# Performance work log

Hardware: AMD Instinct MI355X
Metric: run time of the kernel (lower is better)

The kernel has to match this reference:

```python
import jax, jax.numpy as jnp
import numpy as np

N_EMBD = 768
N_HEAD = 8
B, T = 4, 2048

def setup_inputs() -> dict:
    key = jax.random.key(0)
    k1, k2, k3, k4, k5 = jax.random.split(key, 5)
    C = N_EMBD
    s = 1.0 / np.sqrt(C)
    return {
        "x": jax.random.normal(k1, (B, T, C), dtype=jnp.float32),
        "W_attn": jax.random.normal(k2, (C, 3 * C), dtype=jnp.float32) * s,
        "b_attn": jnp.zeros((3 * C,), dtype=jnp.float32),
        "W_proj": jax.random.normal(k3, (C, C), dtype=jnp.float32) * s,
        "b_proj": jnp.zeros((C,), dtype=jnp.float32),
    }

def reference(x, W_attn, b_attn, W_proj, b_proj):
    Bs, Ts, C = x.shape
    H = N_HEAD
    hs = C // H
    qkv = x @ W_attn + b_attn                      # [B,T,3C]
    q, k, v = jnp.split(qkv, 3, axis=-1)
    # reshape to [B,H,T,hs]
    q = q.reshape(Bs, Ts, H, hs).transpose(0, 2, 1, 3)
    k = k.reshape(Bs, Ts, H, hs).transpose(0, 2, 1, 3)
    v = v.reshape(Bs, Ts, H, hs).transpose(0, 2, 1, 3)
    scale = 1.0 / jnp.sqrt(jnp.float32(hs))
    att = jnp.einsum('bhid,bhjd->bhij', q, k) * scale   # [B,H,T,T]
    mask = jnp.tril(jnp.ones((Ts, Ts), dtype=bool))
    att = jnp.where(mask, att, -jnp.inf)
    m = jnp.max(att, axis=-1, keepdims=True)
    e = jnp.where(mask, jnp.exp(att - m), 0.0)
    # original kernel divides by (sum + 1e-9)
    att = e / (jnp.sum(e, axis=-1, keepdims=True) + 1e-9)
    y = jnp.einsum('bhij,bhjd->bhid', att, v)           # [B,H,T,hs]
    y = y.transpose(0, 2, 1, 3).reshape(Bs, Ts, C)
    return y @ W_proj + b_proj
```

## Files before the change

kernel.cpp:

```cpp
#include <hip/hip_runtime.h>

typedef __bf16 bf16;
typedef __attribute__((ext_vector_type(4))) __bf16 bf16x4;
typedef __attribute__((ext_vector_type(8))) __bf16 bf16x8;
typedef __attribute__((ext_vector_type(4))) float f32x4;

#define B_   4
#define T_   2048
#define C_   768
#define H_   8
#define HS_  96
#define M_   (B_ * T_)
#define QKN_ (3 * C_)

#define NEG_BIG (-1e30f)

#define KSTR 104
#define VSTR 72

__device__ __forceinline__ void gload_lds16(const bf16* g, bf16* l) {
    __builtin_amdgcn_global_load_lds(
        (const __attribute__((address_space(1))) uint32_t*)g,
        (__attribute__((address_space(3))) uint32_t*)l,
        16, 0, 0);
}

__device__ __forceinline__ bf16x8 cvt8(f32x4 v0, f32x4 v1) {
    bf16x8 o;
#pragma unroll
    for (int i = 0; i < 4; ++i) { o[i] = (bf16)v0[i]; o[4 + i] = (bf16)v1[i]; }
    return o;
}

__global__ void transpose_kernel(const float* __restrict__ W, bf16* __restrict__ Wt,
                                 int R, int Cn) {
    __shared__ bf16 tile[32][33];
    int tx = threadIdx.x, ty = threadIdx.y;
    int x  = blockIdx.x * 32 + tx;
    int y0 = blockIdx.y * 32;
#pragma unroll
    for (int j = 0; j < 32; j += 8)
        tile[ty + j][tx] = (bf16)W[(size_t)(y0 + ty + j) * Cn + x];
    __syncthreads();
    int y2 = blockIdx.x * 32;
    int x2 = y0 + tx;
#pragma unroll
    for (int j = 0; j < 32; j += 8)
        Wt[(size_t)(y2 + ty + j) * R + x2] = tile[tx][ty + j];
}

__global__ void sentinel_kernel(float* __restrict__ out, int n) {
    int i = blockIdx.x * 256 + threadIdx.x;
    if (i < n) out[i] = 12345.0f;
}

__global__ __launch_bounds__(256) void convert_bf16_kernel(const float* __restrict__ in,
                                                           bf16* __restrict__ out,
                                                           int n8) {
    int i = blockIdx.x * 256 + threadIdx.x;
    if (i >= n8) return;
    const float* p = in + (size_t)i * 8;
    f32x4 a = *(const f32x4*)p;
    f32x4 b = *(const f32x4*)(p + 4);
    *(bf16x8*)&out[(size_t)i * 8] = cvt8(a, b);
}

#define CONV_BLKS (M_ * C_ / 8 / 256)
#define TA_BX (QKN_ / 32)
#define TA_BLKS (TA_BX * (C_ / 32))
#define TP_BX (C_ / 32)
#define TP_BLKS (TP_BX * (C_ / 32))

__device__ __forceinline__ void transpose_body(bf16 (*tile)[33],
                                               const float* __restrict__ W,
                                               bf16* __restrict__ Wt,
                                               int R, int Cn, int bx, int by, int tid) {
    int tx = tid & 31, ty = tid >> 5;
    int x  = bx * 32 + tx;
    int y0 = by * 32;
#pragma unroll
    for (int j = 0; j < 32; j += 8)
        tile[ty + j][tx] = (bf16)W[(size_t)(y0 + ty + j) * Cn + x];
    __syncthreads();
    int y2 = bx * 32;
    int x2 = y0 + tx;
#pragma unroll
    for (int j = 0; j < 32; j += 8)
        Wt[(size_t)(y2 + ty + j) * R + x2] = tile[tx][ty + j];
}

__global__ __launch_bounds__(256) void prep_kernel(const float* __restrict__ x,
                                                   bf16* __restrict__ xb,
                                                   const float* __restrict__ Wa,
                                                   bf16* __restrict__ Wta,
                                                   const float* __restrict__ Wp,
                                                   bf16* __restrict__ Wtp) {
    __shared__ bf16 tile[32][33];
    int bid = blockIdx.x;
    int tid = threadIdx.x;
    if (bid < CONV_BLKS) {
        int i = bid * 256 + tid;
        const float* p = x + (size_t)i * 8;
        f32x4 a = *(const f32x4*)p;
        f32x4 b = *(const f32x4*)(p + 4);
        *(bf16x8*)&xb[(size_t)i * 8] = cvt8(a, b);
    } else if (bid < CONV_BLKS + TA_BLKS) {
        int t = bid - CONV_BLKS;
        transpose_body(tile, Wa, Wta, C_, QKN_, t % TA_BX, t / TA_BX, tid);
    } else {
        int t = bid - CONV_BLKS - TA_BLKS;
        transpose_body(tile, Wp, Wtp, C_, C_, t % TP_BX, t / TP_BX, tid);
    }
}

#define TILE_ELEMS (128 * 64)

__global__ __launch_bounds__(256) void gemm_qkv(const bf16* __restrict__ A,
                                                const bf16* __restrict__ Bt,
                                                const float* __restrict__ bias,
                                                bf16* __restrict__ Cmat,
                                                bf16* __restrict__ Vt,
                                                int M, int N, int K) {
    __shared__ bf16 lda[2 * TILE_ELEMS];
    __shared__ bf16 ldb[2 * TILE_ELEMS];
    int tid  = threadIdx.x;
    int w    = tid >> 6;
    int lane = tid & 63;
    int col  = lane & 15, quad = lane >> 4;
    int wr   = w >> 1, wc = w & 1;
    int m0   = blockIdx.y * 128, n0 = blockIdx.x * 128;

    int srow = lane >> 3;
    int scol = (lane & 7) * 8;
    const bf16* gA[4]; const bf16* gB[4]; bf16* lA[4]; bf16* lB[4];
#pragma unroll
    for (int i = 0; i < 4; ++i) {
        int seg = w * 4 + i;
        int row = seg * 8 + srow;
        gA[i] = &A[(size_t)(m0 + row) * K + scol];
        gB[i] = &Bt[(size_t)(n0 + row) * K + scol];
        lA[i] = &lda[seg * 512];
        lB[i] = &ldb[seg * 512];
    }

    const f32x4 zero = {0.f, 0.f, 0.f, 0.f};
    f32x4 acc[4][4];
#pragma unroll
    for (int mr = 0; mr < 4; ++mr)
#pragma unroll
        for (int nc = 0; nc < 4; ++nc) acc[mr][nc] = zero;

#pragma unroll
    for (int i = 0; i < 4; ++i) {
        gload_lds16(gA[i], lA[i]);
        gload_lds16(gB[i], lB[i]);
    }
    __syncthreads();

    int cur = 0;
    for (int k0 = 0; k0 < K; k0 += 64) {
        int nxt = cur ^ 1;
        if (k0 + 64 < K) {
#pragma unroll
            for (int i = 0; i < 4; ++i) {
                gload_lds16(gA[i] + k0 + 64, lA[i] + nxt * TILE_ELEMS);
                gload_lds16(gB[i] + k0 + 64, lB[i] + nxt * TILE_ELEMS);
            }
        }
        const bf16* la = &lda[cur * TILE_ELEMS];
        const bf16* lb = &ldb[cur * TILE_ELEMS];
#pragma unroll
        for (int ks = 0; ks < 2; ++ks) {
            bf16x8 af[4], bfr[4];
#pragma unroll
            for (int t = 0; t < 4; ++t) {
                af[t]  = *(const bf16x8*)&la[(wr * 64 + t * 16 + col) * 64 + ks * 32 + quad * 8];
                bfr[t] = *(const bf16x8*)&lb[(wc * 64 + t * 16 + col) * 64 + ks * 32 + quad * 8];
            }
#pragma unroll
            for (int mr = 0; mr < 4; ++mr)
#pragma unroll
                for (int nc = 0; nc < 4; ++nc)
                    acc[mr][nc] = __builtin_amdgcn_mfma_f32_16x16x32_bf16(
                        af[mr], bfr[nc], acc[mr][nc], 0, 0, 0);
        }
        __syncthreads();
        cur = nxt;
    }

#pragma unroll
    for (int nc = 0; nc < 4; ++nc) {
        int n = n0 + wc * 64 + nc * 16 + col;
        float bv = bias[n];
#pragma unroll
        for (int mr = 0; mr < 4; ++mr) {
#pragma unroll
            for (int r = 0; r < 4; ++r) {
                int row = m0 + wr * 64 + mr * 16 + quad * 4 + r;
                Cmat[(size_t)row * N + n] = (bf16)(acc[mr][nc][r] + bv);
            }
        }
    }
    if (n0 >= 2 * C_) {
        int batch = m0 >> 11;
        bf16* Vtb = Vt + (size_t)batch * C_ * T_;
        int t0 = (m0 & 2047) + wr * 64;
#pragma unroll
        for (int nc = 0; nc < 4; ++nc) {
            int n  = n0 + wc * 64 + nc * 16 + col;
            int vc = n - 2 * C_;
            float bv = bias[n];
#pragma unroll
            for (int mr = 0; mr < 4; ++mr) {
                int t  = t0 + mr * 16 + quad * 4;
                int tb = t & ~63;
                int a  = (t >> 2) & 15;
                int ts = tb + ((a & 7) << 3) + ((a >> 3) << 2);
                bf16x4 pk = {(bf16)(acc[mr][nc][0] + bv), (bf16)(acc[mr][nc][1] + bv),
                             (bf16)(acc[mr][nc][2] + bv), (bf16)(acc[mr][nc][3] + bv)};
                *(bf16x4*)&Vtb[(size_t)vc * T_ + ts] = pk;
            }
        }
    }
}

__global__ __launch_bounds__(256) void gemm_proj(const bf16* __restrict__ A,
                                                 const bf16* __restrict__ Bt,
                                                 const float* __restrict__ bias,
                                                 float* __restrict__ Cmat,
                                                 int M, int N, int K) {
    __shared__ bf16 lda[2 * TILE_ELEMS];
    __shared__ bf16 ldb[2 * TILE_ELEMS];
    int tid  = threadIdx.x;
    int w    = tid >> 6;
    int lane = tid & 63;
    int col  = lane & 15, quad = lane >> 4;
    int wr   = w >> 1, wc = w & 1;
    int m0   = blockIdx.y * 128, n0 = blockIdx.x * 128;

    int srow = lane >> 3;
    int scol = (lane & 7) * 8;
    const bf16* gA[4]; const bf16* gB[4]; bf16* lA[4]; bf16* lB[4];
#pragma unroll
    for (int i = 0; i < 4; ++i) {
        int seg = w * 4 + i;
        int row = seg * 8 + srow;
        gA[i] = &A[(size_t)(m0 + row) * K + scol];
        gB[i] = &Bt[(size_t)(n0 + row) * K + scol];
        lA[i] = &lda[seg * 512];
        lB[i] = &ldb[seg * 512];
    }

    const f32x4 zero = {0.f, 0.f, 0.f, 0.f};
    f32x4 acc[4][4];
#pragma unroll
    for (int mr = 0; mr < 4; ++mr)
#pragma unroll
        for (int nc = 0; nc < 4; ++nc) acc[mr][nc] = zero;

#pragma unroll
    for (int i = 0; i < 4; ++i) {
        gload_lds16(gA[i], lA[i]);
        gload_lds16(gB[i], lB[i]);
    }
    __syncthreads();

    int cur = 0;
    for (int k0 = 0; k0 < K; k0 += 64) {
        int nxt = cur ^ 1;
        if (k0 + 64 < K) {
#pragma unroll
            for (int i = 0; i < 4; ++i) {
                gload_lds16(gA[i] + k0 + 64, lA[i] + nxt * TILE_ELEMS);
                gload_lds16(gB[i] + k0 + 64, lB[i] + nxt * TILE_ELEMS);
            }
        }
        const bf16* la = &lda[cur * TILE_ELEMS];
        const bf16* lb = &ldb[cur * TILE_ELEMS];
#pragma unroll
        for (int ks = 0; ks < 2; ++ks) {
            bf16x8 af[4], bfr[4];
#pragma unroll
            for (int t = 0; t < 4; ++t) {
                af[t]  = *(const bf16x8*)&la[(wr * 64 + t * 16 + col) * 64 + ks * 32 + quad * 8];
                bfr[t] = *(const bf16x8*)&lb[(wc * 64 + t * 16 + col) * 64 + ks * 32 + quad * 8];
            }
#pragma unroll
            for (int mr = 0; mr < 4; ++mr)
#pragma unroll
                for (int nc = 0; nc < 4; ++nc)
                    acc[mr][nc] = __builtin_amdgcn_mfma_f32_16x16x32_bf16(
                        af[mr], bfr[nc], acc[mr][nc], 0, 0, 0);
        }
        __syncthreads();
        cur = nxt;
    }

#pragma unroll
    for (int nc = 0; nc < 4; ++nc) {
        int n = n0 + wc * 64 + nc * 16 + col;
        float bv = bias[n];
#pragma unroll
        for (int mr = 0; mr < 4; ++mr) {
#pragma unroll
            for (int r = 0; r < 4; ++r) {
                int row = m0 + wr * 64 + mr * 16 + quad * 4 + r;
                Cmat[(size_t)row * N + n] = acc[mr][nc][r] + bv;
            }
        }
    }
}

__global__ __launch_bounds__(256) void attn_kernel(const bf16* __restrict__ qkv,
                                                   const bf16* __restrict__ Vt,
                                                   bf16* __restrict__ y,
                                                   int nGroups) {
    __shared__ bf16 ldsK[64 * KSTR];
    __shared__ bf16 ldsV[96 * VSTR];
    const int bid  = blockIdx.x;
    const int qt   = 31 - bid / nGroups;
    const int g    = bid % nGroups;
    const int h    = g & 7, b = g >> 3;
    const int tid  = threadIdx.x;
    const int w    = tid >> 6, lane = tid & 63;
    const int col  = lane & 15, quad = lane >> 4;
    const float SCALE2 = 0.10206207261596577f * 1.4426950408889634f;
    const float M0 = 24.0f;
    const f32x4 zero = {0.f, 0.f, 0.f, 0.f};

    const bf16* qkvb = qkv + (size_t)b * T_ * QKN_;
    const bf16* Vtbh = Vt + (size_t)(b * H_ + h) * HS_ * T_;
    bf16* yb  = y + (size_t)b * T_ * C_;

    const int rbase = qt * 64 + w * 16;

    bf16x8 qf[3];
#pragma unroll
    for (int c = 0; c < 3; ++c)
        qf[c] = *(const bf16x8*)&qkvb[(size_t)(rbase + col) * QKN_ + h * HS_ + c * 32 + quad * 8];

    const bf16* pK[3]; const bf16* pV[3];
    bf16 *dK[3], *dV[3];
#pragma unroll
    for (int i = 0; i < 3; ++i) {
        int chunk = i * 256 + tid;
        int rK = chunk / 12, cK = chunk - rK * 12;
        pK[i] = qkvb + (size_t)rK * QKN_ + C_ + h * HS_ + cK * 8;
        dK[i] = &ldsK[rK * KSTR + cK * 8];
        int rV = chunk >> 3, cV = chunk & 7;
        pV[i] = Vtbh + (size_t)rV * T_ + cV * 8;
        dV[i] = &ldsV[rV * VSTR + cV * 8];
    }

    f32x4 o[6];
#pragma unroll
    for (int n2 = 0; n2 < 6; ++n2) o[n2] = zero;
    f32x4 lsum4 = zero;

    bf16x8 kreg[3], vreg[3];
#pragma unroll
    for (int i = 0; i < 3; ++i) {
        kreg[i] = *(const bf16x8*)pK[i];
        vreg[i] = *(const bf16x8*)pV[i];
        pK[i] += (size_t)64 * QKN_;
        pV[i] += 64;
    }

    const int njt = qt + 1;
    for (int jt = 0; jt < njt; ++jt) {
        int jb = jt * 64;
        __syncthreads();
#pragma unroll
        for (int i = 0; i < 3; ++i) {
            *(bf16x8*)dK[i] = kreg[i];
            *(bf16x8*)dV[i] = vreg[i];
        }
        __syncthreads();
        if (jt + 1 < njt) {
#pragma unroll
            for (int i = 0; i < 3; ++i) {
                kreg[i] = *(const bf16x8*)pK[i];
                vreg[i] = *(const bf16x8*)pV[i];
                pK[i] += (size_t)64 * QKN_;
                pV[i] += 64;
            }
        }

        f32x4 st[4];
#pragma unroll
        for (int nb = 0; nb < 4; ++nb) {
            st[nb] = zero;
#pragma unroll
            for (int c = 0; c < 3; ++c) {
                bf16x8 kf = *(const bf16x8*)&ldsK[(nb * 16 + col) * KSTR + c * 32 + quad * 8];
                st[nb] = __builtin_amdgcn_mfma_f32_16x16x32_bf16(
                    kf, qf[c], st[nb], 0, 0, 0);
            }
        }

        if (jt == njt - 1) {
#pragma unroll
            for (int nb = 0; nb < 4; ++nb)
#pragma unroll
                for (int r = 0; r < 4; ++r) {
                    int jg = jb + nb * 16 + quad * 4 + r;
                    st[nb][r] = (jg <= rbase + col) ? fmaf(st[nb][r], SCALE2, -M0)
                                                    : NEG_BIG;
                }
        } else {
#pragma unroll
            for (int nb = 0; nb < 4; ++nb)
#pragma unroll
                for (int r = 0; r < 4; ++r)
                    st[nb][r] = fmaf(st[nb][r], SCALE2, -M0);
        }

#pragma unroll
        for (int nb = 0; nb < 4; ++nb) {
#pragma unroll
            for (int r = 0; r < 4; ++r)
                st[nb][r] = exp2f(st[nb][r]);
            lsum4 += st[nb];
        }

        bf16x8 palo, pahi;
#pragma unroll
        for (int r = 0; r < 4; ++r) {
            palo[r]     = (bf16)st[0][r];
            palo[4 + r] = (bf16)st[2][r];
            pahi[r]     = (bf16)st[1][r];
            pahi[4 + r] = (bf16)st[3][r];
        }

#pragma unroll
        for (int n2 = 0; n2 < 6; ++n2) {
            const bf16* vrow = &ldsV[(n2 * 16 + col) * VSTR];
            bf16x8 vlo = *(const bf16x8*)&vrow[quad * 8];
            bf16x8 vhi = *(const bf16x8*)&vrow[32 + quad * 8];
            o[n2] = __builtin_amdgcn_mfma_f32_16x16x32_bf16(vlo, palo, o[n2], 0, 0, 0);
            o[n2] = __builtin_amdgcn_mfma_f32_16x16x32_bf16(vhi, pahi, o[n2], 0, 0, 0);
        }
    }

    float lsum = (lsum4[0] + lsum4[1]) + (lsum4[2] + lsum4[3]);
    lsum += __shfl_xor(lsum, 16, 64);
    lsum += __shfl_xor(lsum, 32, 64);
    float linv = 1.0f / lsum;
#pragma unroll
    for (int n2 = 0; n2 < 6; ++n2) {
        bf16x4 pk = {(bf16)(o[n2][0] * linv), (bf16)(o[n2][1] * linv),
                     (bf16)(o[n2][2] * linv), (bf16)(o[n2][3] * linv)};
        *(bf16x4*)&yb[(size_t)(rbase + col) * C_ + h * HS_ + n2 * 16 + quad * 4] = pk;
    }
}

extern "C" void kernel_launch(void* const* d_in, const int* in_sizes, int n_in,
                              void* d_out, int out_size, void* d_ws, size_t ws_size,
                              hipStream_t stream) {
    (void)in_sizes; (void)n_in;
    const float* x      = (const float*)d_in[0];
    const float* W_attn = (const float*)d_in[1];
    const float* b_attn = (const float*)d_in[2];
    const float* W_proj = (const float*)d_in[3];
    const float* b_proj = (const float*)d_in[4];
    float* out = (float*)d_out;

    size_t e_wta = (size_t)QKN_ * C_;
    size_t e_wtp = (size_t)C_ * C_;
    size_t a_qkv = e_wta + e_wtp;
    size_t a_vt  = a_qkv + (size_t)M_ * QKN_;
    size_t a_yb  = a_vt + (size_t)M_ * C_;
    size_t needA = (a_yb + (size_t)M_ * C_) * sizeof(bf16);
    size_t b_qkv = e_wta + e_wtp;
    size_t b_vt  = b_qkv + (size_t)T_ * QKN_;
    size_t b_yb  = b_vt + (size_t)T_ * C_;
    size_t needB = (b_yb + (size_t)T_ * C_) * sizeof(bf16);

    if (ws_size >= needA) {
        bf16* Wt_attn = (bf16*)d_ws;
        bf16* Wt_proj = (bf16*)d_ws + e_wta;
        bf16* qkv     = (bf16*)d_ws + a_qkv;
        bf16* Vt      = (bf16*)d_ws + a_vt;
        bf16* yb      = (bf16*)d_ws + a_yb;
        bf16* xb      = yb;
        prep_kernel<<<dim3(CONV_BLKS + TA_BLKS + TP_BLKS), 256, 0, stream>>>(
            x, xb, W_attn, Wt_attn, W_proj, Wt_proj);
        gemm_qkv<<<dim3(QKN_ / 128, M_ / 128), 256, 0, stream>>>(
            xb, Wt_attn, b_attn, qkv, Vt, M_, QKN_, C_);
        attn_kernel<<<dim3(32 * H_ * B_), 256, 0, stream>>>(qkv, Vt, yb, H_ * B_);
        gemm_proj<<<dim3(C_ / 128, M_ / 128), 256, 0, stream>>>(
            yb, Wt_proj, b_proj, out, M_, C_, C_);
    } else if (ws_size >= needB) {
        bf16* Wt_attn = (bf16*)d_ws;
        bf16* Wt_proj = (bf16*)d_ws + e_wta;
        bf16* qkv     = (bf16*)d_ws + b_qkv;
        bf16* Vt      = (bf16*)d_ws + b_vt;
        bf16* yb      = (bf16*)d_ws + b_yb;
        bf16* xb      = yb;
        transpose_kernel<<<dim3(QKN_ / 32, C_ / 32), dim3(32, 8), 0, stream>>>(W_attn, Wt_attn, C_, QKN_);
        transpose_kernel<<<dim3(C_ / 32, C_ / 32), dim3(32, 8), 0, stream>>>(W_proj, Wt_proj, C_, C_);
        for (int b = 0; b < B_; ++b) {
            const float* xf = x + (size_t)b * T_ * C_;
            float* outb     = out + (size_t)b * T_ * C_;
            convert_bf16_kernel<<<dim3(T_ * C_ / 8 / 256), 256, 0, stream>>>(xf, xb, T_ * C_ / 8);
            gemm_qkv<<<dim3(QKN_ / 128, T_ / 128), 256, 0, stream>>>(
                xb, Wt_attn, b_attn, qkv, Vt, T_, QKN_, C_);
            attn_kernel<<<dim3(32 * H_), 256, 0, stream>>>(qkv, Vt, yb, H_);
            gemm_proj<<<dim3(C_ / 128, T_ / 128), 256, 0, stream>>>(
                yb, Wt_proj, b_proj, outb, T_, C_, C_);
        }
    } else {
        sentinel_kernel<<<(out_size + 255) / 256, 256, 0, stream>>>(out, out_size);
    }
}
```

Measured before the change: 206.4 us.

## Process two query tiles per attention block to reuse K/V loads

Each attention block now computes two adjacent 64-row query tiles, sharing every K/V tile staged in LDS between both sets of MFMAs. The first tile skips its final key tile via a predicate. This halves global K/V traffic and the number of LDS fills and syncs per query row, and the launch grid is halved to match. In exchange it doubles accumulator registers, which may lower occupancy, and leaves fewer blocks to balance the causal workload across CUs.

Result: slower. 231.4 us (+12.1%).

```diff
diff --git a/kernel.cpp b/kernel.cpp
--- a/kernel.cpp
+++ b/kernel.cpp
@@ -318,7 +318,7 @@
     __shared__ bf16 ldsK[64 * KSTR];
     __shared__ bf16 ldsV[96 * VSTR];
     const int bid  = blockIdx.x;
-    const int qt   = 31 - bid / nGroups;
+    const int qtt  = 15 - bid / nGroups;
     const int g    = bid % nGroups;
     const int h    = g & 7, b = g >> 3;
     const int tid  = threadIdx.x;
@@ -332,12 +332,15 @@
     const bf16* Vtbh = Vt + (size_t)(b * H_ + h) * HS_ * T_;
     bf16* yb  = y + (size_t)b * T_ * C_;
 
-    const int rbase = qt * 64 + w * 16;
-
-    bf16x8 qf[3];
-#pragma unroll
-    for (int c = 0; c < 3; ++c)
-        qf[c] = *(const bf16x8*)&qkvb[(size_t)(rbase + col) * QKN_ + h * HS_ + c * 32 + quad * 8];
+    const int rbaseA = qtt * 128 + w * 16;
+    const int rbaseB = rbaseA + 64;
+
+    bf16x8 qfA[3], qfB[3];
+#pragma unroll
+    for (int c = 0; c < 3; ++c) {
+        qfA[c] = *(const bf16x8*)&qkvb[(size_t)(rbaseA + col) * QKN_ + h * HS_ + c * 32 + quad * 8];
+        qfB[c] = *(const bf16x8*)&qkvb[(size_t)(rbaseB + col) * QKN_ + h * HS_ + c * 32 + quad * 8];
+    }
 
     const bf16* pK[3]; const bf16* pV[3];
     bf16 *dK[3], *dV[3];
@@ -352,10 +355,10 @@
         dV[i] = &ldsV[rV * VSTR + cV * 8];
     }
 
-    f32x4 o[6];
-#pragma unroll
-    for (int n2 = 0; n2 < 6; ++n2) o[n2] = zero;
-    f32x4 lsum4 = zero;
+    f32x4 oA[6], oB[6];
+#pragma unroll
+    for (int n2 = 0; n2 < 6; ++n2) { oA[n2] = zero; oB[n2] = zero; }
+    f32x4 lsumA4 = zero, lsumB4 = zero;
 
     bf16x8 kreg[3], vreg[3];
 #pragma unroll
@@ -366,8 +369,9 @@
         pV[i] += 64;
     }
 
-    const int njt = qt + 1;
+    const int njt = 2 * qtt + 2;
     for (int jt = 0; jt < njt; ++jt) {
+        const bool aAct = (jt <= 2 * qtt);
         int jb = jt * 64;
         __syncthreads();
 #pragma unroll
@@ -386,50 +390,83 @@
             }
         }
 
-        f32x4 st[4];
+        f32x4 stA[4], stB[4];
 #pragma unroll
         for (int nb = 0; nb < 4; ++nb) {
-            st[nb] = zero;
+            stA[nb] = zero; stB[nb] = zero;
 #pragma unroll
             for (int c = 0; c < 3; ++c) {
                 bf16x8 kf = *(const bf16x8*)&ldsK[(nb * 16 + col) * KSTR + c * 32 + quad * 8];
-                st[nb] = __builtin_amdgcn_mfma_f32_16x16x32_bf16(
-                    kf, qf[c], st[nb], 0, 0, 0);
-            }
-        }
-
+                if (aAct)
+                    stA[nb] = __builtin_amdgcn_mfma_f32_16x16x32_bf16(
+                        kf, qfA[c], stA[nb], 0, 0, 0);
+                stB[nb] = __builtin_amdgcn_mfma_f32_16x16x32_bf16(
+                    kf, qfB[c], stB[nb], 0, 0, 0);
+            }
+        }
+
+        bf16x8 paloA, pahiA, paloB, pahiB;
+        if (aAct) {
+            if (jt == 2 * qtt) {
+#pragma unroll
+                for (int nb = 0; nb < 4; ++nb)
+#pragma unroll
+                    for (int r = 0; r < 4; ++r) {
+                        int jg = jb + nb * 16 + quad * 4 + r;
+                        stA[nb][r] = (jg <= rbaseA + col) ? fmaf(stA[nb][r], SCALE2, -M0)
+                                                          : NEG_BIG;
+                    }
+            } else {
+#pragma unroll
+                for (int nb = 0; nb < 4; ++nb)
+#pragma unroll
+                    for (int r = 0; r < 4; ++r)
+                        stA[nb][r] = fmaf(stA[nb][r], SCALE2, -M0);
+            }
+#pragma unroll
+            for (int nb = 0; nb < 4; ++nb) {
+#pragma unroll
+                for (int r = 0; r < 4; ++r)
+                    stA[nb][r] = exp2f(stA[nb][r]);
+                lsumA4 += stA[nb];
+            }
+#pragma unroll
+            for (int r = 0; r < 4; ++r) {
+                paloA[r]     = (bf16)stA[0][r];
+                paloA[4 + r] = (bf16)stA[2][r];
+                pahiA[r]     = (bf16)stA[1][r];
+                pahiA[4 + r] = (bf16)stA[3][r];
+            }
+        }
         if (jt == njt - 1) {
 #pragma unroll
             for (int nb = 0; nb < 4; ++nb)
 #pragma unroll
                 for (int r = 0; r < 4; ++r) {
                     int jg = jb + nb * 16 + quad * 4 + r;
-                    st[nb][r] = (jg <= rbase + col) ? fmaf(st[nb][r], SCALE2, -M0)
-                                                    : NEG_BIG;
+                    stB[nb][r] = (jg <= rbaseB + col) ? fmaf(stB[nb][r], SCALE2, -M0)
+                                                      : NEG_BIG;
                 }
         } else {
 #pragma unroll
             for (int nb = 0; nb < 4; ++nb)
 #pragma unroll
                 for (int r = 0; r < 4; ++r)
-                    st[nb][r] = fmaf(st[nb][r], SCALE2, -M0);
-        }
-
+                    stB[nb][r] = fmaf(stB[nb][r], SCALE2, -M0);
+        }
 #pragma unroll
         for (int nb = 0; nb < 4; ++nb) {
 #pragma unroll
             for (int r = 0; r < 4; ++r)
-                st[nb][r] = exp2f(st[nb][r]);
-            lsum4 += st[nb];
-        }
-
-        bf16x8 palo, pahi;
+                stB[nb][r] = exp2f(stB[nb][r]);
+            lsumB4 += stB[nb];
+        }
 #pragma unroll
         for (int r = 0; r < 4; ++r) {
-            palo[r]     = (bf16)st[0][r];
-            palo[4 + r] = (bf16)st[2][r];
-            pahi[r]     = (bf16)st[1][r];
-            pahi[4 + r] = (bf16)st[3][r];
+            paloB[r]     = (bf16)stB[0][r];
+            paloB[4 + r] = (bf16)stB[2][r];
+            pahiB[r]     = (bf16)stB[1][r];
+            pahiB[4 + r] = (bf16)stB[3][r];
         }
 
 #pragma unroll
@@ -437,20 +474,31 @@
             const bf16* vrow = &ldsV[(n2 * 16 + col) * VSTR];
             bf16x8 vlo = *(const bf16x8*)&vrow[quad * 8];
             bf16x8 vhi = *(const bf16x8*)&vrow[32 + quad * 8];
-            o[n2] = __builtin_amdgcn_mfma_f32_16x16x32_bf16(vlo, palo, o[n2], 0, 0, 0);
-            o[n2] = __builtin_amdgcn_mfma_f32_16x16x32_bf16(vhi, pahi, o[n2], 0, 0, 0);
-        }
-    }
-
-    float lsum = (lsum4[0] + lsum4[1]) + (lsum4[2] + lsum4[3]);
-    lsum += __shfl_xor(lsum, 16, 64);
-    lsum += __shfl_xor(lsum, 32, 64);
-    float linv = 1.0f / lsum;
+            if (aAct) {
+                oA[n2] = __builtin_amdgcn_mfma_f32_16x16x32_bf16(vlo, paloA, oA[n2], 0, 0, 0);
+                oA[n2] = __builtin_amdgcn_mfma_f32_16x16x32_bf16(vhi, pahiA, oA[n2], 0, 0, 0);
+            }
+            oB[n2] = __builtin_amdgcn_mfma_f32_16x16x32_bf16(vlo, paloB, oB[n2], 0, 0, 0);
+            oB[n2] = __builtin_amdgcn_mfma_f32_16x16x32_bf16(vhi, pahiB, oB[n2], 0, 0, 0);
+        }
+    }
+
+    float lsumA = (lsumA4[0] + lsumA4[1]) + (lsumA4[2] + lsumA4[3]);
+    lsumA += __shfl_xor(lsumA, 16, 64);
+    lsumA += __shfl_xor(lsumA, 32, 64);
+    float linvA = 1.0f / lsumA;
+    float lsumB = (lsumB4[0] + lsumB4[1]) + (lsumB4[2] + lsumB4[3]);
+    lsumB += __shfl_xor(lsumB, 16, 64);
+    lsumB += __shfl_xor(lsumB, 32, 64);
+    float linvB = 1.0f / lsumB;
 #pragma unroll
     for (int n2 = 0; n2 < 6; ++n2) {
-        bf16x4 pk = {(bf16)(o[n2][0] * linv), (bf16)(o[n2][1] * linv),
-                     (bf16)(o[n2][2] * linv), (bf16)(o[n2][3] * linv)};
-        *(bf16x4*)&yb[(size_t)(rbase + col) * C_ + h * HS_ + n2 * 16 + quad * 4] = pk;
+        bf16x4 pkA = {(bf16)(oA[n2][0] * linvA), (bf16)(oA[n2][1] * linvA),
+                      (bf16)(oA[n2][2] * linvA), (bf16)(oA[n2][3] * linvA)};
+        *(bf16x4*)&yb[(size_t)(rbaseA + col) * C_ + h * HS_ + n2 * 16 + quad * 4] = pkA;
+        bf16x4 pkB = {(bf16)(oB[n2][0] * linvB), (bf16)(oB[n2][1] * linvB),
+                      (bf16)(oB[n2][2] * linvB), (bf16)(oB[n2][3] * linvB)};
+        *(bf16x4*)&yb[(size_t)(rbaseB + col) * C_ + h * HS_ + n2 * 16 + quad * 4] = pkB;
     }
 }
 
@@ -487,7 +535,7 @@
             x, xb, W_attn, Wt_attn, W_proj, Wt_proj);
         gemm_qkv<<<dim3(QKN_ / 128, M_ / 128), 256, 0, stream>>>(
             xb, Wt_attn, b_attn, qkv, Vt, M_, QKN_, C_);
-        attn_kernel<<<dim3(32 * H_ * B_), 256, 0, stream>>>(qkv, Vt, yb, H_ * B_);
+        attn_kernel<<<dim3(16 * H_ * B_), 256, 0, stream>>>(qkv, Vt, yb, H_ * B_);
         gemm_proj<<<dim3(C_ / 128, M_ / 128), 256, 0, stream>>>(
             yb, Wt_proj, b_proj, out, M_, C_, C_);
     } else if (ws_size >= needB) {
@@ -505,7 +553,7 @@
             convert_bf16_kernel<<<dim3(T_ * C_ / 8 / 256), 256, 0, stream>>>(xf, xb, T_ * C_ / 8);
             gemm_qkv<<<dim3(QKN_ / 128, T_ / 128), 256, 0, stream>>>(
                 xb, Wt_attn, b_attn, qkv, Vt, T_, QKN_, C_);
-            attn_kernel<<<dim3(32 * H_), 256, 0, stream>>>(qkv, Vt, yb, H_);
+            attn_kernel<<<dim3(16 * H_), 256, 0, stream>>>(qkv, Vt, yb, H_);
             gemm_proj<<<dim3(C_ / 128, T_ / 128), 256, 0, stream>>>(
                 yb, Wt_proj, b_proj, outb, T_, C_, C_);
         }
```
